# Kernel tuning notes

Hardware: AMD Instinct MI355X
Metric: run time of the kernel (lower is better)

## Reference

```python
import jax, jax.numpy as jnp
import numpy as np

NS, NV, HE = 16, 8, 32          # scalar channels, vector (l=1) channels, edge hidden
D = NS + 3 * NV                  # flat irreps feature dim = 40
WN = NS*NS + NV*NS + NS*NV + NV*NV + NV*NV  # per-edge TP weight numel = 640
N_NODES, N_EDGES = 10000, 160000
C110 = 1.0 / np.sqrt(3.0)        # CG norm for 1o x 1o -> 0e (dot)
C111 = 1.0 / np.sqrt(2.0)        # CG norm for 1o x 1o -> 1o (cross)
EPS = 1e-5
_OFF = np.cumsum([0, NS*NS, NV*NS, NS*NV, NV*NV, NV*NV])


def _split(x):
    return x[:, :NS], x[:, NS:].reshape(x.shape[0], NV, 3)


def _flat(s, v):
    return jnp.concatenate([s, v.reshape(v.shape[0], -1)], axis=-1)


def _irreps_linear(x, Ws, Wv):
    s, v = _split(x)
    return s @ Ws, jnp.einsum('nid,io->nod', v, Wv)


def _mlp(x, w1, b1, w2, b2):
    return jax.nn.relu(x @ w1 + b1) @ w2 + b2


def _tp(x_s, x_v, sh, w):
    # equivariant tensor product (feat 16x0e+8x1o) x (sh 1x0e+1x1o) -> (16x0e+8x1o)
    E = x_s.shape[0]
    sh_s, sh_v = sh[:, 0], sh[:, 1:4]
    w1 = w[:, _OFF[0]:_OFF[1]].reshape(E, NS, NS)  # 0e x 0e -> 0e
    w2 = w[:, _OFF[1]:_OFF[2]].reshape(E, NV, NS)  # 1o x 1o -> 0e (dot)
    w3 = w[:, _OFF[2]:_OFF[3]].reshape(E, NS, NV)  # 0e x 1o -> 1o
    w4 = w[:, _OFF[3]:_OFF[4]].reshape(E, NV, NV)  # 1o x 0e -> 1o
    w5 = w[:, _OFF[4]:_OFF[5]].reshape(E, NV, NV)  # 1o x 1o -> 1o (cross)
    dot = jnp.einsum('eid,ed->ei', x_v, sh_v)
    cross = jnp.cross(x_v, sh_v[:, None, :])
    out_s = (jnp.einsum('eio,ei->eo', w1, x_s * sh_s[:, None])
             + C110 * jnp.einsum('eio,ei->eo', w2, dot))
    out_v = (jnp.einsum('eio,ei,ed->eod', w3, x_s, sh_v)
             + jnp.einsum('eio,eid->eod', w4, x_v * sh_s[:, None, None])
             + C111 * jnp.einsum('eio,eid->eod', w5, cross))
    return out_s, out_v


def _batchnorm(x, w_s, b_s, w_v):
    # e3nn-style BatchNorm: standard BN on scalars, norm-normalization on vectors
    s, v = _split(x)
    mu, var = s.mean(0), s.var(0)
    s = (s - mu) / jnp.sqrt(var + EPS) * w_s + b_s
    norm = (v * v).mean(-1).mean(0)  # [NV]
    v = v / jnp.sqrt(norm + EPS)[None, :, None] * w_v[None, :, None]
    return _flat(s, v)


def setup_inputs() -> dict:
    key = jax.random.key(0)
    ks = jax.random.split(key, 12)
    g = lambda i, shape, sc=1.0: jax.random.normal(ks[i], shape, jnp.float32) * sc
    return {
        'atom_features': g(0, (N_NODES, D)),
        'edge_features': g(1, (N_EDGES, HE)),
        'edge_sh': g(2, (N_EDGES, 4)),
        'Wq_s': g(3, (NS, NS), 1.0 / np.sqrt(NS)),
        'Wq_v': g(4, (NV, NV), 1.0 / np.sqrt(NV)),
        'k_w1': g(5, (HE, HE), 1.0 / np.sqrt(HE)), 'k_b1': jnp.zeros((HE,), jnp.float32),
        'k_w2': g(6, (HE, WN), 1.0 / np.sqrt(HE)), 'k_b2': jnp.zeros((WN,), jnp.float32),
        'v_w1': g(7, (HE, HE), 1.0 / np.sqrt(HE)), 'v_b1': jnp.zeros((HE,), jnp.float32),
        'v_w2': g(8, (HE, WN), 1.0 / np.sqrt(HE)), 'v_b2': jnp.zeros((WN,), jnp.float32),
        'bn_w_s': jnp.ones((NS,), jnp.float32), 'bn_b_s': jnp.zeros((NS,), jnp.float32),
        'bn_w_v': jnp.ones((NV,), jnp.float32),
        'edge_index': jax.random.randint(ks[9], (2, N_EDGES), 0, N_NODES),
    }


def reference(atom_features, edge_features, edge_sh, Wq_s, Wq_v,
              k_w1, k_b1, k_w2, k_b2, v_w1, v_b1, v_w2, v_b2,
              bn_w_s, bn_b_s, bn_w_v, edge_index):
    edge_dst, edge_src = edge_index[0], edge_index[1]
    q = _flat(*_irreps_linear(atom_features, Wq_s, Wq_v))[edge_src]     # [E, D]
    x_s, x_v = _split(atom_features[edge_dst])
    k = _flat(*_tp(x_s, x_v, edge_sh, _mlp(edge_features, k_w1, k_b1, k_w2, k_b2)))
    v = _flat(*_tp(x_s, x_v, edge_sh, _mlp(edge_features, v_w1, v_b1, v_w2, v_b2)))
    attn = jnp.sum(q * k, axis=-1)                                       # [E]
    m = jax.ops.segment_max(attn, edge_src, num_segments=N_NODES)
    m = jnp.where(jnp.isfinite(m), m, 0.0)
    e = jnp.exp(attn - m[edge_src])
    denom = jax.ops.segment_sum(e, edge_src, num_segments=N_NODES)
    a = e / denom[edge_src]
    upd = jax.ops.segment_sum(v * a[:, None], edge_src, num_segments=N_NODES)
    out = _batchnorm(atom_features + upd, bn_w_s, bn_b_s, bn_w_v)
    return out, edge_features
```

## Files before the change

### kernel.cpp

```cpp
#include <hip/hip_runtime.h>
#include <hip/hip_bf16.h>

typedef unsigned short u16;
typedef unsigned int u32;
typedef _Float16 h16;

#define NNODES 10000
#define NEDGES 160000

#define C110 0.57735026918962576f
#define C111 0.70710678118654752f

typedef __attribute__((ext_vector_type(8))) _Float16 half8;
typedef __attribute__((ext_vector_type(4))) float f32x4;

__device__ int   g_isf32;
__device__ float g_q[NNODES * 40];
__device__ float g_x[NNODES * 40];
__device__ float g_attn[NEDGES];
__device__ float g_stats[40];
__device__ float g_vbuf[(size_t)NEDGES * 40];
__device__ u32   g_m8[8 * NNODES];
__device__ u32   g_cnt8[8 * NNODES];
__device__ int   g_bucket[(size_t)NNODES * 128];
__device__ h16   g_w1hk[1024], g_w1lk[1024], g_w1hv[1024], g_w1lv[1024];
__device__ __align__(16) h16 g_w2k[640 * 32];
__device__ __align__(16) h16 g_w2v[640 * 32];
__device__ float g_b1k[32], g_b1v[32], g_b2k[640], g_b2v[640];

__device__ __forceinline__ float bf2f(u16 v) {
    return __uint_as_float(((u32)v) << 16);
}
__device__ __forceinline__ u32 f2bfbits(float f) {
    u32 u = __float_as_uint(f);
    u32 r = 0x7FFFu + ((u >> 16) & 1u);
    return (u + r) >> 16;
}
__device__ __forceinline__ u32 pack2(float a, float b) {
    return f2bfbits(a) | (f2bfbits(b) << 16);
}
__device__ __forceinline__ u32 encf(float f) {
    u32 u = __float_as_uint(f);
    return (u & 0x80000000u) ? ~u : (u | 0x80000000u);
}
__device__ __forceinline__ float decf(u32 u) {
    return (u & 0x80000000u) ? __uint_as_float(u & 0x7FFFFFFFu) : __uint_as_float(~u);
}
__device__ __forceinline__ float ldx(const void* p, size_t i, int f32) {
    return f32 ? ((const float*)p)[i] : bf2f(((const u16*)p)[i]);
}
__device__ __forceinline__ void split2h(float v, h16& hi, h16& lo) {
    h16 h = (h16)v;
    hi = h;
    lo = (h16)(v - (float)h);
}
__device__ __forceinline__ void gld16(const void* g, void* l) {
    __builtin_amdgcn_global_load_lds(
        (__attribute__((address_space(1))) void*)(uintptr_t)g,
        (__attribute__((address_space(3))) void*)l, 16, 0, 0);
}

__global__ __launch_bounds__(256) void k_pre(
    const void* __restrict__ atom, const void* __restrict__ Wqs,
    const void* __restrict__ Wqv,
    const void* __restrict__ kw1, const void* __restrict__ kb1,
    const void* __restrict__ kw2, const void* __restrict__ kb2,
    const void* __restrict__ vw1, const void* __restrict__ vb1,
    const void* __restrict__ vw2, const void* __restrict__ vb2) {
    __shared__ int sF32;
    __shared__ float sW[320];
    const int tid = threadIdx.x;
    const u16* atom16 = (const u16*)atom;

    if (tid < 64) {
        int cnt = 0;
        #pragma unroll 4
        for (int j = tid * 16; j < tid * 16 + 16; ++j) {
            float ve = bf2f(atom16[2 * j]);
            float ae = fabsf(ve);
            if (ve == 0.f || (ae > 9.3e-13f && ae < 1.1e12f)) cnt++;
        }
        cnt += __shfl_xor(cnt, 1);  cnt += __shfl_xor(cnt, 2);
        cnt += __shfl_xor(cnt, 4);  cnt += __shfl_xor(cnt, 8);
        cnt += __shfl_xor(cnt, 16); cnt += __shfl_xor(cnt, 32);
        if (tid == 0) {
            int r = (cnt < 716) ? 1 : 0;
            sF32 = r;
            if (blockIdx.x == 0) g_isf32 = r;
        }
    }
    __syncthreads();
    const int f32 = sF32;

    int i = blockIdx.x * 256 + tid;
    if (i < 8 * NNODES) {
        g_cnt8[i] = 0u;
        g_m8[i] = 0x007FFFFFu;
    }
    if (i < 40) g_stats[i] = 0.f;

    if (blockIdx.x >= 40 && blockIdx.x < 120) {
        int t = i - 10240;
        if (t < 640 * 32) {
            int k = t / 640, n = t - k * 640;
            g_w2k[n * 32 + k] = (h16)ldx(kw2, t, f32);
            g_w2v[n * 32 + k] = (h16)ldx(vw2, t, f32);
        }
        if (t < 1024) {
            int s = t >> 5, tt = t & 31;
            split2h(ldx(kw1, t, f32), g_w1hk[tt * 32 + s], g_w1lk[tt * 32 + s]);
            split2h(ldx(vw1, t, f32), g_w1hv[tt * 32 + s], g_w1lv[tt * 32 + s]);
        }
        if (t < 640) { g_b2k[t] = ldx(kb2, t, f32); g_b2v[t] = ldx(vb2, t, f32); }
        if (t < 32)  { g_b1k[t] = ldx(kb1, t, f32); g_b1v[t] = ldx(vb1, t, f32); }
    } else if (blockIdx.x < 40) {
        sW[tid] = ldx(Wqs, tid, f32);
        if (tid < 64) sW[256 + tid] = ldx(Wqv, tid, f32);
        __syncthreads();
        int n = i;
        if (n >= NNODES) return;
        float x[40];
        if (f32) {
            const float4* ap = (const float4*)((const float*)atom + (size_t)n * 40);
            #pragma unroll
            for (int c = 0; c < 10; ++c) {
                float4 v = ap[c];
                x[c*4+0] = v.x; x[c*4+1] = v.y; x[c*4+2] = v.z; x[c*4+3] = v.w;
            }
        } else {
            #pragma unroll 1
            for (int c = 0; c < 40; ++c) x[c] = bf2f(((const u16*)atom)[(size_t)n * 40 + c]);
        }
        float qs[16];
        #pragma unroll
        for (int o = 0; o < 16; ++o) qs[o] = 0.f;
        #pragma unroll 1
        for (int ii = 0; ii < 16; ++ii) {
            float ai = x[ii];
            #pragma unroll
            for (int o = 0; o < 16; ++o) qs[o] = fmaf(ai, sW[ii * 16 + o], qs[o]);
        }
        float qv[24];
        #pragma unroll
        for (int k = 0; k < 24; ++k) qv[k] = 0.f;
        #pragma unroll 1
        for (int ii = 0; ii < 8; ++ii) {
            float a0 = x[16 + 3*ii + 0], a1 = x[16 + 3*ii + 1], a2 = x[16 + 3*ii + 2];
            #pragma unroll
            for (int o = 0; o < 8; ++o) {
                float wv = sW[256 + ii * 8 + o];
                qv[o*3+0] = fmaf(a0, wv, qv[o*3+0]);
                qv[o*3+1] = fmaf(a1, wv, qv[o*3+1]);
                qv[o*3+2] = fmaf(a2, wv, qv[o*3+2]);
            }
        }
        float* qp = g_q + (size_t)n * 40;
        #pragma unroll
        for (int o = 0; o < 16; ++o) qp[o] = qs[o];
        #pragma unroll
        for (int k = 0; k < 24; ++k) qp[16 + k] = qv[k];
    }
}

#define ACCS 41

#define STAGE(cc, WK, WV) do { \
    gld16((const char*)g_w2k + (cc)*4096 + w*1024 + lane*16, (char*)(WK) + w*1024); \
    gld16((const char*)g_w2v + (cc)*4096 + w*1024 + lane*16, (char*)(WV) + w*1024); \
} while (0)

#define TILE(nt, WK, WV) do { \
    const int tl_ = (nt) & 3; \
    half8 bk = *(const half8*)((WK) + (tl_*16 + c) * 32 + quad * 8); \
    half8 bv = *(const half8*)((WV) + (tl_*16 + c) * 32 + quad * 8); \
    float bbk = sB2k[(nt)*16 + c], bbv = sB2v[(nt)*16 + c]; \
    f32x4 Ck = {0.f,0.f,0.f,0.f}, Cv = {0.f,0.f,0.f,0.f}; \
    Ck = __builtin_amdgcn_mfma_f32_16x16x32_f16(aflk, bk, Ck, 0, 0, 0); \
    Ck = __builtin_amdgcn_mfma_f32_16x16x32_f16(afhk, bk, Ck, 0, 0, 0); \
    Cv = __builtin_amdgcn_mfma_f32_16x16x32_f16(aflv, bv, Cv, 0, 0, 0); \
    Cv = __builtin_amdgcn_mfma_f32_16x16x32_f16(afhv, bv, Cv, 0, 0, 0); \
    if ((nt) < 16) { \
        f32x4 xf = *(const f32x4*)(smF + (8 + (nt)) * 64 + e0); \
        _Pragma("unroll") \
        for (int r = 0; r < 4; ++r) { float fr = xf[r] * ssf[r]; \
            aSk[r] = fmaf(Ck[r] + bbk, fr, aSk[r]); \
            aSv[r] = fmaf(Cv[r] + bbv, fr, aSv[r]); } \
    } else if ((nt) < 24) { \
        f32x4 f = *(const f32x4*)(smF + ((nt) - 16) * 64 + e0); \
        _Pragma("unroll") \
        for (int r = 0; r < 4; ++r) { \
            aSk[r] = fmaf(Ck[r] + bbk, f[r], aSk[r]); \
            aSv[r] = fmaf(Cv[r] + bbv, f[r], aSv[r]); } \
    } else if ((nt) < 32) { \
        f32x4 f = *(const f32x4*)(smF + (8 + 2*((nt)-24) + ch) * 64 + e0); \
        _Pragma("unroll") \
        for (int r = 0; r < 4; ++r) { \
            aTk[r] = fmaf(Ck[r] + bbk, f[r], aTk[r]); \
            aTv[r] = fmaf(Cv[r] + bbv, f[r], aTv[r]); } \
    } else if ((nt) < 36) { \
        const int i_ = 2*((nt)-32) + ch; \
        _Pragma("unroll") \
        for (int d = 0; d < 3; ++d) { \
            f32x4 f = *(const f32x4*)(smF + (24 + d*8 + i_) * 64 + e0); \
            _Pragma("unroll") \
            for (int r = 0; r < 4; ++r) { \
                aVk[d*4+r] = fmaf(Ck[r] + bbk, f[r], aVk[d*4+r]); \
                aVv[d*4+r] = fmaf(Cv[r] + bbv, f[r], aVv[d*4+r]); } } \
    } else { \
        const int i_ = 2*((nt)-36) + ch; \
        _Pragma("unroll") \
        for (int d = 0; d < 3; ++d) { \
            f32x4 f = *(const f32x4*)(smF + (48 + d*8 + i_) * 64 + e0); \
            _Pragma("unroll") \
            for (int r = 0; r < 4; ++r) { \
                aVk[d*4+r] = fmaf(Ck[r] + bbk, f[r], aVk[d*4+r]); \
                aVv[d*4+r] = fmaf(Cv[r] + bbv, f[r], aVv[d*4+r]); } } \
    } \
} while (0)

#define DO_CHUNK(cc, WK, WV) do { \
    TILE((cc)*4 + 0, WK, WV); \
    TILE((cc)*4 + 1, WK, WV); \
    TILE((cc)*4 + 2, WK, WV); \
    TILE((cc)*4 + 3, WK, WV); \
} while (0)

__global__ __launch_bounds__(256, 4) void k_edge(
    const void* __restrict__ atom, const void* __restrict__ ef,
    const void* __restrict__ sh, const int* __restrict__ ei,
    void* __restrict__ out) {
    __shared__ __align__(16) float smF[76 * 64];
    __shared__ __align__(16) h16 sWkA[2048], sWvA[2048];
    __shared__ __align__(16) h16 sWkB[2048], sWvB[2048];
    __shared__ float sB2k[640], sB2v[640];

    const int f32 = g_isf32;
    const int t = threadIdx.x;
    const int w = t >> 6, lane = t & 63;
    const int quad = lane >> 4, c = lane & 15;
    const int eb = blockIdx.x * 64;
    const int slice = blockIdx.x & 7;

    STAGE(0, sWkA, sWvA);
    for (int i2 = t; i2 < 640; i2 += 256) { sB2k[i2] = g_b2k[i2]; sB2v[i2] = g_b2v[i2]; }

    if (f32) {
        const uint4* s = (const uint4*)ef;
        uint4* d = (uint4*)((char*)out + 1600000u);
        size_t i = (size_t)blockIdx.x * 512 + t;
        d[i] = s[i]; d[i + 256] = s[i + 256];
    } else {
        const uint4* s = (const uint4*)ef;
        uint4* d = (uint4*)((char*)out + 800000u);
        size_t i = (size_t)blockIdx.x * 256 + t;
        d[i] = s[i];
    }

    half8 efh, efl;
    {
        const size_t base = (size_t)(eb + w * 16 + c) * 32 + quad * 8;
        h16 th, tl;
        if (f32) {
            const float4* ep = (const float4*)((const float*)ef + base);
            float4 v0 = ep[0], v1 = ep[1];
            split2h(v0.x, th, tl); efh[0] = th; efl[0] = tl;
            split2h(v0.y, th, tl); efh[1] = th; efl[1] = tl;
            split2h(v0.z, th, tl); efh[2] = th; efl[2] = tl;
            split2h(v0.w, th, tl); efh[3] = th; efl[3] = tl;
            split2h(v1.x, th, tl); efh[4] = th; efl[4] = tl;
            split2h(v1.y, th, tl); efh[5] = th; efl[5] = tl;
            split2h(v1.z, th, tl); efh[6] = th; efl[6] = tl;
            split2h(v1.w, th, tl); efh[7] = th; efl[7] = tl;
        } else {
            const u16* ep = (const u16*)ef + base;
            #pragma unroll
            for (int j = 0; j < 8; ++j) {
                split2h(bf2f(ep[j]), th, tl);
                efh[j] = th; efl[j] = tl;
            }
        }
    }

    if (lane < 16) {
        const int e = w * 16 + lane;
        const int ge = eb + e;
        const int dst = ei[ge];
        float x[40];
        float ss, s0, s1, s2;
        if (f32) {
            const float4* xp = (const float4*)((const float*)atom + (size_t)dst * 40);
            #pragma unroll
            for (int i = 0; i < 10; ++i) {
                float4 v = xp[i];
                x[i*4+0] = v.x; x[i*4+1] = v.y; x[i*4+2] = v.z; x[i*4+3] = v.w;
            }
            float4 s4 = *(const float4*)((const float*)sh + (size_t)ge * 4);
            ss = s4.x; s0 = s4.y; s1 = s4.z; s2 = s4.w;
        } else {
            #pragma unroll
            for (int i = 0; i < 40; ++i) x[i] = bf2f(((const u16*)atom)[(size_t)dst * 40 + i]);
            ss = bf2f(((const u16*)sh)[(size_t)ge*4+0]);
            s0 = bf2f(((const u16*)sh)[(size_t)ge*4+1]);
            s1 = bf2f(((const u16*)sh)[(size_t)ge*4+2]);
            s2 = bf2f(((const u16*)sh)[(size_t)ge*4+3]);
        }
        #pragma unroll
        for (int i = 0; i < 16; ++i)
            smF[(8 + i) * 64 + e] = x[i];
        #pragma unroll
        for (int i = 0; i < 8; ++i) {
            float a0 = x[16+3*i], a1 = x[17+3*i], a2 = x[18+3*i];
            smF[i * 64 + e]        = C110 * (a0*s0 + a1*s1 + a2*s2);
            smF[(24 + i) * 64 + e] = a0 * ss;
            smF[(32 + i) * 64 + e] = a1 * ss;
            smF[(40 + i) * 64 + e] = a2 * ss;
            smF[(48 + i) * 64 + e] = C111 * (a1*s2 - a2*s1);
            smF[(56 + i) * 64 + e] = C111 * (a2*s0 - a0*s2);
            smF[(64 + i) * 64 + e] = C111 * (a0*s1 - a1*s0);
        }
        smF[72*64 + e] = s0; smF[73*64 + e] = s1; smF[74*64 + e] = s2;
        smF[75*64 + e] = ss;
    }

    half8 afhk, aflk, afhv, aflv;
    #pragma unroll
    for (int p = 0; p < 2; ++p) {
        const h16* w1h = p ? g_w1hv : g_w1hk;
        const h16* w1l = p ? g_w1lv : g_w1lk;
        const float* b1 = p ? g_b1v : g_b1k;
        f32x4 H0, H1;
        #pragma unroll
        for (int nt = 0; nt < 2; ++nt) {
            half8 ah = *(const half8*)(w1h + (nt*16 + c) * 32 + quad * 8);
            half8 al = *(const half8*)(w1l + (nt*16 + c) * 32 + quad * 8);
            f32x4 D = {0.f, 0.f, 0.f, 0.f};
            D = __builtin_amdgcn_mfma_f32_16x16x32_f16(al, efh, D, 0, 0, 0);
            D = __builtin_amdgcn_mfma_f32_16x16x32_f16(ah, efl, D, 0, 0, 0);
            D = __builtin_amdgcn_mfma_f32_16x16x32_f16(ah, efh, D, 0, 0, 0);
            #pragma unroll
            for (int r = 0; r < 4; ++r)
                D[r] = fmaxf(D[r] + b1[nt*16 + quad*4 + r], 0.f);
            if (nt == 0) H0 = D; else H1 = D;
        }
        half8 th8, tl8;
        #pragma unroll
        for (int j = 0; j < 8; ++j) {
            int sl = (((2*quad + (j >> 2)) & 3) << 4) + c;
            float v0 = __shfl(H0[j & 3], sl);
            float v1 = __shfl(H1[j & 3], sl);
            float val = (quad < 2) ? v0 : v1;
            h16 hh, ll;
            split2h(val, hh, ll);
            th8[j] = hh; tl8[j] = ll;
        }
        if (p == 0) { afhk = th8; aflk = tl8; }
        else        { afhv = th8; aflv = tl8; }
    }

    const int e0 = w * 16 + quad * 4;
    const int o = c & 7, ch = c >> 3;

    f32x4 ssf = *(const f32x4*)(smF + 75*64 + e0);

    float aSk[4] = {0.f,0.f,0.f,0.f}, aTk[4] = {0.f,0.f,0.f,0.f};
    float aVk[12] = {0.f,0.f,0.f,0.f,0.f,0.f,0.f,0.f,0.f,0.f,0.f,0.f};
    float aSv[4] = {0.f,0.f,0.f,0.f}, aTv[4] = {0.f,0.f,0.f,0.f};
    float aVv[12] = {0.f,0.f,0.f,0.f,0.f,0.f,0.f,0.f,0.f,0.f,0.f,0.f};

    __syncthreads();
    STAGE(1, sWkB, sWvB);  DO_CHUNK(0, sWkA, sWvA);
    __syncthreads();
    STAGE(2, sWkA, sWvA);  DO_CHUNK(1, sWkB, sWvB);
    __syncthreads();
    STAGE(3, sWkB, sWvB);  DO_CHUNK(2, sWkA, sWvA);
    __syncthreads();
    STAGE(4, sWkA, sWvA);  DO_CHUNK(3, sWkB, sWvB);
    __syncthreads();
    STAGE(5, sWkB, sWvB);  DO_CHUNK(4, sWkA, sWvA);
    __syncthreads();
    STAGE(6, sWkA, sWvA);  DO_CHUNK(5, sWkB, sWvB);
    __syncthreads();
    STAGE(7, sWkB, sWvB);  DO_CHUNK(6, sWkA, sWvA);
    __syncthreads();
    STAGE(8, sWkA, sWvA);  DO_CHUNK(7, sWkB, sWvB);
    __syncthreads();
    STAGE(9, sWkB, sWvB);  DO_CHUNK(8, sWkA, sWvA);
    __syncthreads();
    DO_CHUNK(9, sWkB, sWvB);
    __syncthreads();

    float* const accp = smF + w * 656;

    const int el = lane >> 2, part = lane & 3;
    const int ge2 = eb + w * 16 + el;

    #pragma unroll
    for (int r = 0; r < 4; ++r) accp[(quad*4 + r) * ACCS + c] = aSk[r];
    #pragma unroll
    for (int r = 0; r < 4; ++r) aTk[r] += __shfl_xor(aTk[r], 8);
    #pragma unroll
    for (int d = 0; d < 3; ++d)
        #pragma unroll
        for (int r = 0; r < 4; ++r) aVk[d*4+r] += __shfl_xor(aVk[d*4+r], 8);
    if (ch == 0) {
        #pragma unroll
        for (int d = 0; d < 3; ++d) {
            f32x4 sv = *(const f32x4*)(smF + (72 + d) * 64 + e0);
            #pragma unroll
            for (int r = 0; r < 4; ++r)
                accp[(quad*4 + r) * ACCS + 16 + o*3 + d] = aVk[d*4+r] + aTk[r] * sv[r];
        }
    }
    {
        const int src = ei[NEDGES + ge2];
        const float* qp = g_q + (size_t)src * 40 + part * 10;
        const float* ap = accp + el * ACCS + part * 10;
        float partial = 0.f;
        #pragma unroll
        for (int d2 = 0; d2 < 10; ++d2) partial = fmaf(qp[d2], ap[d2], partial);
        partial += __shfl_xor(partial, 1);
        partial += __shfl_xor(partial, 2);
        if (part == 0) {
            g_attn[ge2] = partial;
            atomicMax(&g_m8[slice * NNODES + src], encf(partial));
            u32 pos = atomicAdd(&g_cnt8[slice * NNODES + src], 1u);
            if (pos < 16u) g_bucket[(size_t)src * 128 + slice * 16 + pos] = ge2;
        }
    }

    #pragma unroll
    for (int r = 0; r < 4; ++r) accp[(quad*4 + r) * ACCS + c] = aSv[r];
    #pragma unroll
    for (int r = 0; r < 4; ++r) aTv[r] += __shfl_xor(aTv[r], 8);
    #pragma unroll
    for (int d = 0; d < 3; ++d)
        #pragma unroll
        for (int r = 0; r < 4; ++r) aVv[d*4+r] += __shfl_xor(aVv[d*4+r], 8);
    if (ch == 0) {
        #pragma unroll
        for (int d = 0; d < 3; ++d) {
            f32x4 sv = *(const f32x4*)(smF + (72 + d) * 64 + e0);
            #pragma unroll
            for (int r = 0; r < 4; ++r)
                accp[(quad*4 + r) * ACCS + 16 + o*3 + d] = aVv[d*4+r] + aTv[r] * sv[r];
        }
    }
    {
        float* vb = g_vbuf + (size_t)ge2 * 40 + part * 10;
        const float* ap = accp + el * ACCS + part * 10;
        #pragma unroll
        for (int d2 = 0; d2 < 10; ++d2) vb[d2] = ap[d2];
    }
}

__global__ __launch_bounds__(256) void k_post(const void* __restrict__ atom) {
    __shared__ float part_s[40];
    __shared__ int   sse[4][128];
    __shared__ float ssp[4][128];
    const int f32 = g_isf32;
    const int w = threadIdx.x >> 6;
    const int node = blockIdx.x * 4 + w;
    const int lane = threadIdx.x & 63;
    if (threadIdx.x < 40) part_s[threadIdx.x] = 0.f;
    __syncthreads();

    float m = -__builtin_huge_valf();
    #pragma unroll
    for (int s = 0; s < 8; ++s) m = fmaxf(m, decf(g_m8[s * NNODES + node]));

    float p0 = 0.f, p1 = 0.f;
    int eA = 0, eB = 0;
    {
        const int idx = lane & 15;
        u32 c0 = g_cnt8[(lane >> 4) * NNODES + node];
        if (c0 > 16u) c0 = 16u;
        if ((u32)idx < c0) {
            eA = g_bucket[(size_t)node * 128 + lane];
            p0 = expf(fminf(g_attn[eA] - m, 0.f));
        }
        u32 c1 = g_cnt8[(4 + (lane >> 4)) * NNODES + node];
        if (c1 > 16u) c1 = 16u;
        if ((u32)idx < c1) {
            eB = g_bucket[(size_t)node * 128 + 64 + lane];
            p1 = expf(fminf(g_attn[eB] - m, 0.f));
        }
    }
    float dv = p0 + p1;
    dv += __shfl_xor(dv, 1);  dv += __shfl_xor(dv, 2);
    dv += __shfl_xor(dv, 4);  dv += __shfl_xor(dv, 8);
    dv += __shfl_xor(dv, 16); dv += __shfl_xor(dv, 32);
    const float den = dv;

    const unsigned long long below = (1ull << lane) - 1ull;
    unsigned long long mk0 = __ballot(p0 != 0.f);
    if (p0 != 0.f) {
        int idx = (int)__popcll(mk0 & below);
        sse[w][idx] = eA; ssp[w][idx] = p0;
    }
    int n0 = (int)__popcll(mk0);
    unsigned long long mk1 = __ballot(p1 != 0.f);
    if (p1 != 0.f) {
        int idx = n0 + (int)__popcll(mk1 & below);
        sse[w][idx] = eB; ssp[w][idx] = p1;
    }
    const int n = n0 + (int)__popcll(mk1);

    float a0 = 0.f, a1 = 0.f, a2 = 0.f, a3 = 0.f;
    if (lane < 40) {
        int k = 0;
        for (; k + 4 <= n; k += 4) {
            a0 = fmaf(ssp[w][k+0], g_vbuf[(size_t)sse[w][k+0] * 40 + lane], a0);
            a1 = fmaf(ssp[w][k+1], g_vbuf[(size_t)sse[w][k+1] * 40 + lane], a1);
            a2 = fmaf(ssp[w][k+2], g_vbuf[(size_t)sse[w][k+2] * 40 + lane], a2);
            a3 = fmaf(ssp[w][k+3], g_vbuf[(size_t)sse[w][k+3] * 40 + lane], a3);
        }
        for (; k < n; ++k)
            a0 = fmaf(ssp[w][k], g_vbuf[(size_t)sse[w][k] * 40 + lane], a0);
    }
    float acc = (a0 + a1) + (a2 + a3);

    float inv = (den > 0.f) ? 1.f / den : 0.f;
    float xv = 0.f;
    if (lane < 40) {
        xv = ldx(atom, (size_t)node * 40 + lane, f32) + acc * inv;
        g_x[(size_t)node * 40 + lane] = xv;
    }
    if (lane < 16) {
        atomicAdd(&part_s[lane], xv);
        atomicAdd(&part_s[16 + lane], xv * xv);
    }
    float sq = xv * xv;
    float tri = sq + __shfl_down(sq, 1) + __shfl_down(sq, 2);
    if (lane >= 16 && lane < 40 && ((lane - 16) % 3 == 0))
        atomicAdd(&part_s[32 + (lane - 16) / 3], tri);
    __syncthreads();
    if (threadIdx.x < 40) atomicAdd(&g_stats[threadIdx.x], part_s[threadIdx.x]);
}

__global__ __launch_bounds__(256) void k_out(
    const void* __restrict__ bws, const void* __restrict__ bbs,
    const void* __restrict__ bwv, void* __restrict__ out) {
    __shared__ float spar[40];
    const int f32 = g_isf32;
    int t = threadIdx.x;
    const float invN = 1.f / (float)NNODES;
    if (t < 16) {
        float mu = g_stats[t] * invN;
        float var = fmaxf(g_stats[16 + t] * invN - mu * mu, 0.f);
        float isd = 1.f / sqrtf(var + 1e-5f);
        float sc = ldx(bws, t, f32) * isd;
        spar[t] = sc;
        spar[16 + t] = ldx(bbs, t, f32) - mu * sc;
    } else if (t >= 32 && t < 40) {
        int i = t - 32;
        float norm = g_stats[32 + i] * (invN / 3.f);
        spar[32 + i] = ldx(bwv, i, f32) / sqrtf(norm + 1e-5f);
    }
    __syncthreads();

    int n = blockIdx.x * 256 + t;
    if (n >= NNODES) return;
    const float4* xp4 = (const float4*)(g_x + (size_t)n * 40);
    float xp[40];
    #pragma unroll
    for (int c = 0; c < 10; ++c) {
        float4 v = xp4[c];
        xp[c*4+0] = v.x; xp[c*4+1] = v.y; xp[c*4+2] = v.z; xp[c*4+3] = v.w;
    }
    float res[40];
    #pragma unroll
    for (int c = 0; c < 16; ++c) res[c] = xp[c] * spar[c] + spar[16 + c];
    #pragma unroll
    for (int i = 0; i < 8; ++i) {
        float s = spar[32 + i];
        res[16+3*i+0] = xp[16+3*i+0] * s;
        res[16+3*i+1] = xp[16+3*i+1] * s;
        res[16+3*i+2] = xp[16+3*i+2] * s;
    }
    if (f32) {
        float4* op = (float4*)((float*)out + (size_t)n * 40);
        #pragma unroll
        for (int c = 0; c < 10; ++c)
            op[c] = make_float4(res[c*4+0], res[c*4+1], res[c*4+2], res[c*4+3]);
    } else {
        uint4* op = (uint4*)((u16*)out + (size_t)n * 40);
        #pragma unroll
        for (int c = 0; c < 5; ++c) {
            uint4 r;
            r.x = pack2(res[c*8+0], res[c*8+1]);
            r.y = pack2(res[c*8+2], res[c*8+3]);
            r.z = pack2(res[c*8+4], res[c*8+5]);
            r.w = pack2(res[c*8+6], res[c*8+7]);
            op[c] = r;
        }
    }
}

extern "C" void kernel_launch(void* const* d_in, const int* in_sizes, int n_in,
                              void* d_out, int out_size, void* d_ws, size_t ws_size,
                              hipStream_t stream) {
    const void* atom = d_in[0];
    const void* ef   = d_in[1];
    const void* sh   = d_in[2];
    const void* Wqs  = d_in[3];
    const void* Wqv  = d_in[4];
    const void* kw1  = d_in[5];
    const void* kb1  = d_in[6];
    const void* kw2  = d_in[7];
    const void* kb2  = d_in[8];
    const void* vw1  = d_in[9];
    const void* vb1  = d_in[10];
    const void* vw2  = d_in[11];
    const void* vb2  = d_in[12];
    const void* bws  = d_in[13];
    const void* bbs  = d_in[14];
    const void* bwv  = d_in[15];
    const int*  ei   = (const int*)d_in[16];

    k_pre <<<320, 256, 0, stream>>>(atom, Wqs, Wqv, kw1, kb1, kw2, kb2,
                                    vw1, vb1, vw2, vb2);
    k_edge<<<2500, 256, 0, stream>>>(atom, ef, sh, ei, d_out);
    k_post<<<2500, 256, 0, stream>>>(atom);
    k_out <<<40, 256, 0, stream>>>(bws, bbs, bwv, d_out);
}
```

Before: 218.9 us.

## Drop split-fp16 low MFMA, fold bias into accumulator, move edge copy to k_pre

```diff
diff --git a/kernel.cpp b/kernel.cpp
--- a/kernel.cpp
+++ b/kernel.cpp
@@ -18,7 +18,7 @@
 __device__ float g_q[NNODES * 40];
 __device__ float g_x[NNODES * 40];
 __device__ float g_attn[NEDGES];
-__device__ float g_stats[40];
+__device__ float g_stats8[8][40];
 __device__ float g_vbuf[(size_t)NEDGES * 40];
 __device__ u32   g_m8[8 * NNODES];
 __device__ u32   g_cnt8[8 * NNODES];
@@ -54,6 +54,12 @@
     hi = h;
     lo = (h16)(v - (float)h);
 }
+__device__ __forceinline__ void unp8(uint4 v, float* x) {
+    x[0] = bf2f((u16)(v.x & 0xffffu)); x[1] = bf2f((u16)(v.x >> 16));
+    x[2] = bf2f((u16)(v.y & 0xffffu)); x[3] = bf2f((u16)(v.y >> 16));
+    x[4] = bf2f((u16)(v.z & 0xffffu)); x[5] = bf2f((u16)(v.z >> 16));
+    x[6] = bf2f((u16)(v.w & 0xffffu)); x[7] = bf2f((u16)(v.w >> 16));
+}
 __device__ __forceinline__ void gld16(const void* g, void* l) {
     __builtin_amdgcn_global_load_lds(
         (__attribute__((address_space(1))) void*)(uintptr_t)g,
@@ -66,7 +72,8 @@
     const void* __restrict__ kw1, const void* __restrict__ kb1,
     const void* __restrict__ kw2, const void* __restrict__ kb2,
     const void* __restrict__ vw1, const void* __restrict__ vb1,
-    const void* __restrict__ vw2, const void* __restrict__ vb2) {
+    const void* __restrict__ vw2, const void* __restrict__ vb2,
+    const void* __restrict__ ef, void* __restrict__ out) {
     __shared__ int sF32;
     __shared__ float sW[320];
     const int tid = threadIdx.x;
@@ -97,7 +104,7 @@
         g_cnt8[i] = 0u;
         g_m8[i] = 0x007FFFFFu;
     }
-    if (i < 40) g_stats[i] = 0.f;
+    if (i < 320) ((float*)g_stats8)[i] = 0.f;
 
     if (blockIdx.x >= 40 && blockIdx.x < 120) {
         int t = i - 10240;
@@ -128,8 +135,9 @@
                 x[c*4+0] = v.x; x[c*4+1] = v.y; x[c*4+2] = v.z; x[c*4+3] = v.w;
             }
         } else {
-            #pragma unroll 1
-            for (int c = 0; c < 40; ++c) x[c] = bf2f(((const u16*)atom)[(size_t)n * 40 + c]);
+            const uint4* ap = (const uint4*)((const u16*)atom + (size_t)n * 40);
+            #pragma unroll
+            for (int c = 0; c < 5; ++c) unp8(ap[c], x + c * 8);
         }
         float qs[16];
         #pragma unroll
@@ -159,6 +167,19 @@
         for (int o = 0; o < 16; ++o) qp[o] = qs[o];
         #pragma unroll
         for (int k = 0; k < 24; ++k) qp[16 + k] = qv[k];
+    } else {
+        const size_t b = blockIdx.x - 120;
+        if (f32) {
+            const uint4* s = (const uint4*)ef;
+            uint4* d = (uint4*)((char*)out + 1600000u);
+            for (size_t idx = b * 256 + tid; idx < 1280000u; idx += 200u * 256u)
+                d[idx] = s[idx];
+        } else {
+            const uint4* s = (const uint4*)ef;
+            uint4* d = (uint4*)((char*)out + 800000u);
+            for (size_t idx = b * 256 + tid; idx < 640000u; idx += 200u * 256u)
+                d[idx] = s[idx];
+        }
     }
 }
 
@@ -174,29 +195,28 @@
     half8 bk = *(const half8*)((WK) + (tl_*16 + c) * 32 + quad * 8); \
     half8 bv = *(const half8*)((WV) + (tl_*16 + c) * 32 + quad * 8); \
     float bbk = sB2k[(nt)*16 + c], bbv = sB2v[(nt)*16 + c]; \
-    f32x4 Ck = {0.f,0.f,0.f,0.f}, Cv = {0.f,0.f,0.f,0.f}; \
-    Ck = __builtin_amdgcn_mfma_f32_16x16x32_f16(aflk, bk, Ck, 0, 0, 0); \
+    f32x4 Ck = {bbk, bbk, bbk, bbk}; \
+    f32x4 Cv = {bbv, bbv, bbv, bbv}; \
     Ck = __builtin_amdgcn_mfma_f32_16x16x32_f16(afhk, bk, Ck, 0, 0, 0); \
-    Cv = __builtin_amdgcn_mfma_f32_16x16x32_f16(aflv, bv, Cv, 0, 0, 0); \
     Cv = __builtin_amdgcn_mfma_f32_16x16x32_f16(afhv, bv, Cv, 0, 0, 0); \
     if ((nt) < 16) { \
         f32x4 xf = *(const f32x4*)(smF + (8 + (nt)) * 64 + e0); \
         _Pragma("unroll") \
         for (int r = 0; r < 4; ++r) { float fr = xf[r] * ssf[r]; \
-            aSk[r] = fmaf(Ck[r] + bbk, fr, aSk[r]); \
-            aSv[r] = fmaf(Cv[r] + bbv, fr, aSv[r]); } \
+            aSk[r] = fmaf(Ck[r], fr, aSk[r]); \
+            aSv[r] = fmaf(Cv[r], fr, aSv[r]); } \
     } else if ((nt) < 24) { \
         f32x4 f = *(const f32x4*)(smF + ((nt) - 16) * 64 + e0); \
         _Pragma("unroll") \
         for (int r = 0; r < 4; ++r) { \
-            aSk[r] = fmaf(Ck[r] + bbk, f[r], aSk[r]); \
-            aSv[r] = fmaf(Cv[r] + bbv, f[r], aSv[r]); } \
+            aSk[r] = fmaf(Ck[r], f[r], aSk[r]); \
+            aSv[r] = fmaf(Cv[r], f[r], aSv[r]); } \
     } else if ((nt) < 32) { \
         f32x4 f = *(const f32x4*)(smF + (8 + 2*((nt)-24) + ch) * 64 + e0); \
         _Pragma("unroll") \
         for (int r = 0; r < 4; ++r) { \
-            aTk[r] = fmaf(Ck[r] + bbk, f[r], aTk[r]); \
-            aTv[r] = fmaf(Cv[r] + bbv, f[r], aTv[r]); } \
+            aTk[r] = fmaf(Ck[r], f[r], aTk[r]); \
+            aTv[r] = fmaf(Cv[r], f[r], aTv[r]); } \
     } else if ((nt) < 36) { \
         const int i_ = 2*((nt)-32) + ch; \
         _Pragma("unroll") \
@@ -204,8 +224,8 @@
             f32x4 f = *(const f32x4*)(smF + (24 + d*8 + i_) * 64 + e0); \
             _Pragma("unroll") \
             for (int r = 0; r < 4; ++r) { \
-                aVk[d*4+r] = fmaf(Ck[r] + bbk, f[r], aVk[d*4+r]); \
-                aVv[d*4+r] = fmaf(Cv[r] + bbv, f[r], aVv[d*4+r]); } } \
+                aVk[d*4+r] = fmaf(Ck[r], f[r], aVk[d*4+r]); \
+                aVv[d*4+r] = fmaf(Cv[r], f[r], aVv[d*4+r]); } } \
     } else { \
         const int i_ = 2*((nt)-36) + ch; \
         _Pragma("unroll") \
@@ -213,8 +233,8 @@
             f32x4 f = *(const f32x4*)(smF + (48 + d*8 + i_) * 64 + e0); \
             _Pragma("unroll") \
             for (int r = 0; r < 4; ++r) { \
-                aVk[d*4+r] = fmaf(Ck[r] + bbk, f[r], aVk[d*4+r]); \
-                aVv[d*4+r] = fmaf(Cv[r] + bbv, f[r], aVv[d*4+r]); } } \
+                aVk[d*4+r] = fmaf(Ck[r], f[r], aVk[d*4+r]); \
+                aVv[d*4+r] = fmaf(Cv[r], f[r], aVv[d*4+r]); } } \
     } \
 } while (0)
 
@@ -243,18 +263,6 @@
 
     STAGE(0, sWkA, sWvA);
     for (int i2 = t; i2 < 640; i2 += 256) { sB2k[i2] = g_b2k[i2]; sB2v[i2] = g_b2v[i2]; }
-
-    if (f32) {
-        const uint4* s = (const uint4*)ef;
-        uint4* d = (uint4*)((char*)out + 1600000u);
-        size_t i = (size_t)blockIdx.x * 512 + t;
-        d[i] = s[i]; d[i + 256] = s[i + 256];
-    } else {
-        const uint4* s = (const uint4*)ef;
-        uint4* d = (uint4*)((char*)out + 800000u);
-        size_t i = (size_t)blockIdx.x * 256 + t;
-        d[i] = s[i];
-    }
 
     half8 efh, efl;
     {
@@ -272,10 +280,12 @@
             split2h(v1.z, th, tl); efh[6] = th; efl[6] = tl;
             split2h(v1.w, th, tl); efh[7] = th; efl[7] = tl;
         } else {
-            const u16* ep = (const u16*)ef + base;
+            uint4 v = *(const uint4*)((const u16*)ef + base);
+            float xe[8];
+            unp8(v, xe);
             #pragma unroll
             for (int j = 0; j < 8; ++j) {
-                split2h(bf2f(ep[j]), th, tl);
+                split2h(xe[j], th, tl);
                 efh[j] = th; efl[j] = tl;
             }
         }
@@ -297,12 +307,12 @@
             float4 s4 = *(const float4*)((const float*)sh + (size_t)ge * 4);
             ss = s4.x; s0 = s4.y; s1 = s4.z; s2 = s4.w;
         } else {
-            #pragma unroll
-            for (int i = 0; i < 40; ++i) x[i] = bf2f(((const u16*)atom)[(size_t)dst * 40 + i]);
-            ss = bf2f(((const u16*)sh)[(size_t)ge*4+0]);
-            s0 = bf2f(((const u16*)sh)[(size_t)ge*4+1]);
-            s1 = bf2f(((const u16*)sh)[(size_t)ge*4+2]);
-            s2 = bf2f(((const u16*)sh)[(size_t)ge*4+3]);
+            const uint4* xp = (const uint4*)((const u16*)atom + (size_t)dst * 40);
+            #pragma unroll
+            for (int i = 0; i < 5; ++i) unp8(xp[i], x + i * 8);
+            uint2 s2v = *(const uint2*)((const u16*)sh + (size_t)ge * 4);
+            ss = bf2f((u16)(s2v.x & 0xffffu)); s0 = bf2f((u16)(s2v.x >> 16));
+            s1 = bf2f((u16)(s2v.y & 0xffffu)); s2 = bf2f((u16)(s2v.y >> 16));
         }
         #pragma unroll
         for (int i = 0; i < 16; ++i)
@@ -322,7 +332,7 @@
         smF[75*64 + e] = ss;
     }
 
-    half8 afhk, aflk, afhv, aflv;
+    half8 afhk, afhv;
     #pragma unroll
     for (int p = 0; p < 2; ++p) {
         const h16* w1h = p ? g_w1hv : g_w1hk;
@@ -342,19 +352,16 @@
                 D[r] = fmaxf(D[r] + b1[nt*16 + quad*4 + r], 0.f);
             if (nt == 0) H0 = D; else H1 = D;
         }
-        half8 th8, tl8;
+        half8 th8;
         #pragma unroll
         for (int j = 0; j < 8; ++j) {
             int sl = (((2*quad + (j >> 2)) & 3) << 4) + c;
             float v0 = __shfl(H0[j & 3], sl);
             float v1 = __shfl(H1[j & 3], sl);
             float val = (quad < 2) ? v0 : v1;
-            h16 hh, ll;
-            split2h(val, hh, ll);
-            th8[j] = hh; tl8[j] = ll;
-        }
-        if (p == 0) { afhk = th8; aflk = tl8; }
-        else        { afhv = th8; aflv = tl8; }
+            th8[j] = (h16)val;
+        }
+        if (p == 0) afhk = th8; else afhv = th8;
     }
 
     const int e0 = w * 16 + quad * 4;
@@ -534,27 +541,36 @@
     if (lane >= 16 && lane < 40 && ((lane - 16) % 3 == 0))
         atomicAdd(&part_s[32 + (lane - 16) / 3], tri);
     __syncthreads();
-    if (threadIdx.x < 40) atomicAdd(&g_stats[threadIdx.x], part_s[threadIdx.x]);
+    if (threadIdx.x < 40)
+        atomicAdd(&g_stats8[blockIdx.x & 7][threadIdx.x], part_s[threadIdx.x]);
 }
 
 __global__ __launch_bounds__(256) void k_out(
     const void* __restrict__ bws, const void* __restrict__ bbs,
     const void* __restrict__ bwv, void* __restrict__ out) {
+    __shared__ float sst[40];
     __shared__ float spar[40];
     const int f32 = g_isf32;
     int t = threadIdx.x;
     const float invN = 1.f / (float)NNODES;
+    if (t < 40) {
+        float s_ = 0.f;
+        #pragma unroll
+        for (int s = 0; s < 8; ++s) s_ += g_stats8[s][t];
+        sst[t] = s_;
+    }
+    __syncthreads();
     if (t < 16) {
-        float mu = g_stats[t] * invN;
-        float var = fmaxf(g_stats[16 + t] * invN - mu * mu, 0.f);
+        float mu = sst[t] * invN;
+        float var = fmaxf(sst[16 + t] * invN - mu * mu, 0.f);
         float isd = 1.f / sqrtf(var + 1e-5f);
         float sc = ldx(bws, t, f32) * isd;
         spar[t] = sc;
         spar[16 + t] = ldx(bbs, t, f32) - mu * sc;
     } else if (t >= 32 && t < 40) {
         int i = t - 32;
-        float norm = g_stats[32 + i] * (invN / 3.f);
-        spar[32 + i] = ldx(bwv, i, f32) / sqrtf(norm + 1e-5f);
+        float norm = sst[t] * (invN / 3.f);
+        spar[t] = ldx(bwv, i, f32) / sqrtf(norm + 1e-5f);
     }
     __syncthreads();
 
@@ -618,7 +634,7 @@
     const int*  ei   = (const int*)d_in[16];
 
     k_pre <<<320, 256, 0, stream>>>(atom, Wqs, Wqv, kw1, kb1, kw2, kb2,
-                                    vw1, vb1, vw2, vb2);
+                                    vw1, vb1, vw2, vb2, ef, d_out);
     k_edge<<<2500, 256, 0, stream>>>(atom, ef, sh, ei, d_out);
     k_post<<<2500, 256, 0, stream>>>(atom);
     k_out <<<40, 256, 0, stream>>>(bws, bbs, bwv, d_out);
```

Result: faster. 196.8 us (-10.1%).
